# Kernel tuning notes

Measured on AMD Instinct MI355X. Metric: run time of the kernel, lower is better.

## Reference

```python
import jax, jax.numpy as jnp
import numpy as np

N = 100000
IN_DIM = 256
HID = 256
EMB = 64
E = 3200000
EPS = 1e-3  # keras BatchNormalization default epsilon


def setup_inputs() -> dict:
    key = jax.random.key(0)
    ks = jax.random.split(key, 8)
    x = jax.random.normal(ks[0], (N, IN_DIM), dtype=jnp.float32)
    edge_row = jax.random.randint(ks[1], (E,), 0, N, dtype=jnp.int32)
    edge_col = jax.random.randint(ks[2], (E,), 0, N, dtype=jnp.int32)
    edge_val = jax.random.uniform(ks[3], (E,), dtype=jnp.float32)
    # glorot-uniform weights
    lim1 = float(np.sqrt(6.0 / (IN_DIM + HID)))
    w1 = jax.random.uniform(ks[4], (IN_DIM, HID), minval=-lim1, maxval=lim1, dtype=jnp.float32)
    lim2 = float(np.sqrt(6.0 / (HID + EMB)))
    w2 = jax.random.uniform(ks[5], (HID, EMB), minval=-lim2, maxval=lim2, dtype=jnp.float32)
    # BN params (inference mode uses moving stats)
    gamma1 = jnp.ones((HID,), jnp.float32)
    beta1 = jnp.zeros((HID,), jnp.float32)
    mean1 = jax.random.normal(ks[6], (HID,), dtype=jnp.float32) * 0.1
    var1 = jnp.ones((HID,), jnp.float32)
    gamma2 = jnp.ones((EMB,), jnp.float32)
    beta2 = jnp.zeros((EMB,), jnp.float32)
    mean2 = jax.random.normal(ks[7], (EMB,), dtype=jnp.float32) * 0.1
    var2 = jnp.ones((EMB,), jnp.float32)
    return dict(x=x, edge_row=edge_row, edge_col=edge_col, edge_val=edge_val,
                w1=w1, w2=w2, gamma1=gamma1, beta1=beta1, mean1=mean1, var1=var1,
                gamma2=gamma2, beta2=beta2, mean2=mean2, var2=var2)


def _spmm(edge_row, edge_col, edge_val, dense):
    # out[i] = sum_{e: row_e == i} val_e * dense[col_e]
    gathered = edge_val[:, None] * dense[edge_col]  # [E, D]
    return jax.ops.segment_sum(gathered, edge_row, num_segments=N)


def _bn_inf(h, gamma, beta, mean, var):
    return (h - mean) * jax.lax.rsqrt(var + EPS) * gamma + beta


def reference(x, edge_row, edge_col, edge_val, w1, w2,
              gamma1, beta1, mean1, var1, gamma2, beta2, mean2, var2):
    # layer 1: A @ (X W1), BN (inference), ReLU; dropout is identity at inference
    h = _spmm(edge_row, edge_col, edge_val, x @ w1)
    h = jax.nn.relu(_bn_inf(h, gamma1, beta1, mean1, var1))
    # layer 2
    z = _spmm(edge_row, edge_col, edge_val, h @ w2)
    z = _bn_inf(z, gamma2, beta2, mean2, var2)
    return z
```

## Files before the change

kernel.cpp:

```cpp
#include <hip/hip_runtime.h>
#include <hip/hip_bf16.h>

constexpr int NN   = 100000;
constexpr int IND  = 256;
constexpr int HIDD = 256;
constexpr int EMBD = 64;
constexpr int EE   = 3200000;
constexpr int CB    = 8;
constexpr int NB    = ((NN - 1) >> CB) + 1;
constexpr int NBP   = 512;
constexpr int CHUNK = 4096;
constexpr int EPT   = CHUNK / 256;
constexpr int NCHUNK = (EE + CHUNK - 1) / CHUNK;
constexpr int GMT    = 8;
constexpr int GROWS  = GMT * 16;
constexpr int GGRID  = (NN + GROWS - 1) / GROWS;
constexpr int APITCH = 264;
#define EPS_BN 1e-3f

typedef short  short8  __attribute__((ext_vector_type(8)));
typedef float  floatx4 __attribute__((ext_vector_type(4)));
typedef float  floatx2 __attribute__((ext_vector_type(2)));

static __device__ __forceinline__ unsigned short f2bf(float f) {
  __hip_bfloat16 b = __float2bfloat16(f);
  union { __hip_bfloat16 b; unsigned short u; } cv;
  cv.b = b;
  return cv.u;
}
static __device__ __forceinline__ float bf2f(unsigned short u) {
  return __uint_as_float(((unsigned)u) << 16);
}
static __device__ __forceinline__ unsigned char f2fp8(float f) {
  return (unsigned char)__builtin_amdgcn_cvt_pk_fp8_f32(f, f, 0, false);
}

__global__ __launch_bounds__(256) void swz_w1_kernel(
    const float* __restrict__ w1, unsigned short* __restrict__ w1s) {
  const int t = blockIdx.x * blockDim.x + threadIdx.x;
  const int lane = t & 63;
  const int f = t >> 6;
  const int kt = f >> 4;
  const int nt = f & 15;
  const int n = nt * 16 + (lane & 15);
#pragma unroll
  for (int j = 0; j < 8; ++j) {
    const int k = kt * 32 + (lane >> 4) * 8 + j;
    w1s[(size_t)(f * 64 + lane) * 8 + j] = f2bf(w1[k * HIDD + n]);
  }
}

__global__ __launch_bounds__(256) void swz_w2_kernel(
    const float* __restrict__ w2, unsigned short* __restrict__ w2s) {
  const int t = blockIdx.x * blockDim.x + threadIdx.x;
  const int lane = t & 63;
  const int f = t >> 6;
  const int kt = f >> 2;
  const int nt = f & 3;
  const int n = nt * 16 + (lane & 15);
#pragma unroll
  for (int j = 0; j < 8; ++j) {
    const int k = kt * 32 + (lane >> 4) * 8 + j;
    w2s[(size_t)(f * 64 + lane) * 8 + j] = f2bf(w2[k * EMBD + n]);
  }
}

__global__ __launch_bounds__(512) void gemm1_mfma(
    const float* __restrict__ x, const unsigned short* __restrict__ w1s,
    unsigned char* __restrict__ h0) {
  __shared__ unsigned short sa[2][16][APITCH];
  const int tid  = threadIdx.x;
  const int lane = tid & 63;
  const int wave = tid >> 6;
  const int quad = lane >> 4;
  const int l15  = lane & 15;
  const short8* w1v = (const short8*)w1s;
  short8 bf[2][8];
#pragma unroll
  for (int nt2 = 0; nt2 < 2; ++nt2)
#pragma unroll
    for (int kt = 0; kt < 8; ++kt)
      bf[nt2][kt] = w1v[(size_t)(kt * 16 + wave * 2 + nt2) * 64 + lane];

  const int mbase = blockIdx.x * GROWS;
  const int srow = tid >> 5;
  const int scol = (tid & 31) * 8;

  auto srcp = [&](int mt) -> const float* {
    int r = mbase + mt * 16 + srow;
    if (r >= NN) r = NN - 1;
    return x + (size_t)r * IND + scol;
  };

  {
    const float* p = srcp(0);
    float4 g0 = *(const float4*)(p);
    float4 g1 = *(const float4*)(p + 4);
    short8 s;
    s[0] = (short)f2bf(g0.x); s[1] = (short)f2bf(g0.y);
    s[2] = (short)f2bf(g0.z); s[3] = (short)f2bf(g0.w);
    s[4] = (short)f2bf(g1.x); s[5] = (short)f2bf(g1.y);
    s[6] = (short)f2bf(g1.z); s[7] = (short)f2bf(g1.w);
    *(short8*)&sa[0][srow][(tid & 31) * 8] = s;
  }

#pragma unroll
  for (int mt = 0; mt < GMT; ++mt) {
    const int cur = mt & 1;
    float4 g0, g1;
    if (mt + 1 < GMT) {
      const float* p = srcp(mt + 1);
      g0 = *(const float4*)(p);
      g1 = *(const float4*)(p + 4);
    }
    __syncthreads();
    floatx4 c0 = {0.f, 0.f, 0.f, 0.f};
    floatx4 c1 = {0.f, 0.f, 0.f, 0.f};
#pragma unroll
    for (int kt = 0; kt < 8; ++kt) {
      short8 a = *(const short8*)&sa[cur][l15][quad * 8 + kt * 32];
      c0 = __builtin_amdgcn_mfma_f32_16x16x32_bf16(a, bf[0][kt], c0, 0, 0, 0);
      c1 = __builtin_amdgcn_mfma_f32_16x16x32_bf16(a, bf[1][kt], c1, 0, 0, 0);
    }
    const int m0 = mbase + mt * 16;
    if (m0 < NN) {
      unsigned char* o = h0 + (size_t)(m0 + quad * 4) * HIDD + wave * 32 + l15;
#pragma unroll
      for (int r = 0; r < 4; ++r) {
        o[(size_t)r * HIDD]      = f2fp8(c0[r]);
        o[(size_t)r * HIDD + 16] = f2fp8(c1[r]);
      }
    }
    if (mt + 1 < GMT) {
      short8 s;
      s[0] = (short)f2bf(g0.x); s[1] = (short)f2bf(g0.y);
      s[2] = (short)f2bf(g0.z); s[3] = (short)f2bf(g0.w);
      s[4] = (short)f2bf(g1.x); s[5] = (short)f2bf(g1.y);
      s[6] = (short)f2bf(g1.z); s[7] = (short)f2bf(g1.w);
      *(short8*)&sa[cur ^ 1][srow][(tid & 31) * 8] = s;
    }
  }
}

__global__ __launch_bounds__(256) void gemm2_mfma(
    const unsigned short* __restrict__ hb, const unsigned short* __restrict__ w2s,
    unsigned char* __restrict__ z0) {
  __shared__ unsigned short sa[2][16][APITCH];
  const int tid  = threadIdx.x;
  const int lane = tid & 63;
  const int wave = tid >> 6;
  const int quad = lane >> 4;
  const int l15  = lane & 15;
  const short8* w2v = (const short8*)w2s;
  short8 bf[8];
#pragma unroll
  for (int kt = 0; kt < 8; ++kt)
    bf[kt] = w2v[(size_t)(kt * 4 + wave) * 64 + lane];

  const int mbase = blockIdx.x * GROWS;
  const int srow = tid >> 4;
  const int scol = (tid & 15) * 16;

  auto srcp = [&](int mt) -> const unsigned short* {
    int r = mbase + mt * 16 + srow;
    if (r >= NN) r = NN - 1;
    return hb + (size_t)r * HIDD + scol;
  };

  {
    const unsigned short* p = srcp(0);
    short8 g0 = *(const short8*)(p);
    short8 g1 = *(const short8*)(p + 8);
    *(short8*)&sa[0][srow][scol]     = g0;
    *(short8*)&sa[0][srow][scol + 8] = g1;
  }

#pragma unroll
  for (int mt = 0; mt < GMT; ++mt) {
    const int cur = mt & 1;
    short8 g0, g1;
    if (mt + 1 < GMT) {
      const unsigned short* p = srcp(mt + 1);
      g0 = *(const short8*)(p);
      g1 = *(const short8*)(p + 8);
    }
    __syncthreads();
    floatx4 c = {0.f, 0.f, 0.f, 0.f};
#pragma unroll
    for (int kt = 0; kt < 8; ++kt) {
      short8 a = *(const short8*)&sa[cur][l15][quad * 8 + kt * 32];
      c = __builtin_amdgcn_mfma_f32_16x16x32_bf16(a, bf[kt], c, 0, 0, 0);
    }
    const int m0 = mbase + mt * 16;
    if (m0 < NN) {
      unsigned char* o = z0 + (size_t)(m0 + quad * 4) * EMBD + wave * 16 + l15;
#pragma unroll
      for (int r = 0; r < 4; ++r) o[(size_t)r * EMBD] = f2fp8(c[r]);
    }
    if (mt + 1 < GMT) {
      *(short8*)&sa[cur ^ 1][srow][scol]     = g0;
      *(short8*)&sa[cur ^ 1][srow][scol + 8] = g1;
    }
  }
}

__global__ __launch_bounds__(256) void histb_kernel(
    const int* __restrict__ row, int* __restrict__ bcnt) {
  __shared__ int lcnt[NB];
  for (int i = threadIdx.x; i < NB; i += 256) lcnt[i] = 0;
  __syncthreads();
  const int base = blockIdx.x * CHUNK;
  const int lim  = min(EE - base, CHUNK);
  for (int i = threadIdx.x; i < lim; i += 256)
    atomicAdd(&lcnt[row[base + i] >> CB], 1);
  __syncthreads();
  for (int i = threadIdx.x; i < NB; i += 256) {
    const int c = lcnt[i];
    if (c) atomicAdd(&bcnt[i * 16], c);
  }
}

__global__ __launch_bounds__(512) void bscan_kernel(
    const int* __restrict__ bcnt, int* __restrict__ bucket_start,
    int* __restrict__ bcur) {
  __shared__ int lds[512];
  int v = (threadIdx.x < NB) ? bcnt[threadIdx.x * 16] : 0;
  lds[threadIdx.x] = v;
  for (int off = 1; off < 512; off <<= 1) {
    __syncthreads();
    int t = (threadIdx.x >= off) ? lds[threadIdx.x - off] : 0;
    __syncthreads();
    lds[threadIdx.x] += t;
  }
  __syncthreads();
  if (threadIdx.x < NB) {
    const int excl = lds[threadIdx.x] - v;
    bucket_start[threadIdx.x] = excl;
    bcur[threadIdx.x * 16] = excl;
  }
  if (threadIdx.x == 0) bucket_start[NB] = EE;
}

__global__ __launch_bounds__(256) void partA_kernel(
    const int* __restrict__ row, const int* __restrict__ col,
    const float* __restrict__ val, int* __restrict__ bcur,
    unsigned long long* __restrict__ staged) {
  __shared__ unsigned long long sbuf[CHUNK];
  __shared__ int cnt[NBP];
  __shared__ int scn[NBP];
  __shared__ int cur[NB];
  __shared__ int gofs[NB];
  const int base = blockIdx.x * CHUNK;
  const int lim  = min(EE - base, CHUNK);
  for (int i = threadIdx.x; i < NBP; i += 256) cnt[i] = 0;
  __syncthreads();
  unsigned long long rec[EPT];
  int bkt[EPT];
#pragma unroll
  for (int j = 0; j < EPT; ++j) {
    const int idx = threadIdx.x + j * 256;
    bkt[j] = -1;
    if (idx < lim) {
      const int e = base + idx;
      const int r = row[e];
      const int c = col[e];
      const unsigned short v = f2bf(val[e]);
      rec[j] = ((unsigned long long)r << 33) | ((unsigned long long)c << 16) | v;
      bkt[j] = r >> CB;
      atomicAdd(&cnt[bkt[j]], 1);
    }
  }
  __syncthreads();
  for (int i = threadIdx.x; i < NBP; i += 256) scn[i] = cnt[i];
  __syncthreads();
  for (int off = 1; off < NBP; off <<= 1) {
    const int i0 = threadIdx.x, i1 = threadIdx.x + 256;
    const int t0 = (i0 >= off) ? scn[i0 - off] : 0;
    const int t1 = (i1 >= off) ? scn[i1 - off] : 0;
    __syncthreads();
    scn[i0] += t0;
    scn[i1] += t1;
    __syncthreads();
  }
  for (int b = threadIdx.x; b < NB; b += 256) cur[b] = scn[b] - cnt[b];
  __syncthreads();
#pragma unroll
  for (int j = 0; j < EPT; ++j)
    if (bkt[j] >= 0) {
      const int p = atomicAdd(&cur[bkt[j]], 1);
      sbuf[p] = rec[j];
    }
  __syncthreads();
  for (int b = threadIdx.x; b < NB; b += 256) {
    const int c = cnt[b];
    const int g = (c > 0) ? atomicAdd(&bcur[b * 16], c) : 0;
    gofs[b] = g - (scn[b] - c);
  }
  __syncthreads();
  for (int s = threadIdx.x; s < lim; s += 256) {
    const unsigned long long rc = sbuf[s];
    const int b = (int)(rc >> (33 + CB));
    staged[(size_t)(gofs[b] + s)] = rc;
  }
}

__global__ __launch_bounds__(256) void partB_kernel(
    const int* __restrict__ bucket_start,
    const unsigned long long* __restrict__ staged,
    int2* __restrict__ edges, int* __restrict__ row_start) {
  __shared__ int cnt[1 << CB];
  __shared__ int ofs[1 << CB];
  const int b  = blockIdx.x;
  const int r0 = b << CB;
  const int rn = min(NN - r0, 1 << CB);
  const int s  = bucket_start[b];
  const int e  = bucket_start[b + 1];
  cnt[threadIdx.x] = 0;
  __syncthreads();
  const unsigned* hi = (const unsigned*)staged;
  for (int p = s + threadIdx.x; p < e; p += 256) {
    const unsigned hw = hi[2 * p + 1];
    const int r = (int)((hw >> 1) & 0x1FFFF);
    atomicAdd(&cnt[r - r0], 1);
  }
  __syncthreads();
  const int v = cnt[threadIdx.x];
  ofs[threadIdx.x] = v;
  for (int off = 1; off < 256; off <<= 1) {
    __syncthreads();
    const int t = (threadIdx.x >= off) ? ofs[threadIdx.x - off] : 0;
    __syncthreads();
    ofs[threadIdx.x] += t;
  }
  __syncthreads();
  const int excl = ofs[threadIdx.x] - v;
  if ((int)threadIdx.x < rn) row_start[r0 + threadIdx.x] = s + excl;
  if (b == NB - 1 && threadIdx.x == 0) row_start[NN] = e;
  __syncthreads();
  cnt[threadIdx.x] = s + excl;
  __syncthreads();
  for (int p = s + threadIdx.x; p < e; p += 256) {
    const unsigned long long rc = staged[p];
    const int r = (int)(rc >> 33);
    const int c = (int)((rc >> 16) & 0x1FFFF);
    const float vv = bf2f((unsigned short)(rc & 0xFFFF));
    const int q = atomicAdd(&cnt[r - r0], 1);
    int2 pk; pk.x = c << 6; pk.y = __float_as_int(vv);
    edges[q] = pk;
  }
}

__global__ __launch_bounds__(256, 8) void spmm1_kernel(
    const unsigned char* __restrict__ h0, const int* __restrict__ row_start,
    const int2* __restrict__ edges,
    const float* __restrict__ gamma, const float* __restrict__ beta,
    const float* __restrict__ mean, const float* __restrict__ var,
    unsigned short* __restrict__ h) {
  const int row  = (blockIdx.x * blockDim.x + threadIdx.x) >> 6;
  const int lane = threadIdx.x & 63;
  const int grp  = lane >> 4;
  const int t    = lane & 15;
  const int t16  = t * 16;
  const int s = row_start[row];
  const int e = row_start[row + 1];
  floatx2 acc[8];
#pragma unroll
  for (int j = 0; j < 8; ++j) acc[j] = floatx2{0.f, 0.f};

  const int ebulk = s + ((e - s) & ~15);
  int p = s;
  for (; p < ebulk; p += 16) {
    unsigned coff[4];
    float    vv4[4];
#pragma unroll
    for (int k = 0; k < 4; ++k) {
      const int2 er = edges[p + k * 4 + grp];
      coff[k] = (unsigned)er.x;
      vv4[k]  = __int_as_float(er.y);
    }
    uint4 gg[4];
#pragma unroll
    for (int k = 0; k < 4; ++k)
      gg[k] = *(const uint4*)(h0 + (size_t)coff[k] * 4 + t16);
#pragma unroll
    for (int k = 0; k < 4; ++k) {
      const floatx2 v2 = {vv4[k], vv4[k]};
      acc[0] += __builtin_amdgcn_cvt_pk_f32_fp8(gg[k].x, false) * v2;
      acc[1] += __builtin_amdgcn_cvt_pk_f32_fp8(gg[k].x, true)  * v2;
      acc[2] += __builtin_amdgcn_cvt_pk_f32_fp8(gg[k].y, false) * v2;
      acc[3] += __builtin_amdgcn_cvt_pk_f32_fp8(gg[k].y, true)  * v2;
      acc[4] += __builtin_amdgcn_cvt_pk_f32_fp8(gg[k].z, false) * v2;
      acc[5] += __builtin_amdgcn_cvt_pk_f32_fp8(gg[k].z, true)  * v2;
      acc[6] += __builtin_amdgcn_cvt_pk_f32_fp8(gg[k].w, false) * v2;
      acc[7] += __builtin_amdgcn_cvt_pk_f32_fp8(gg[k].w, true)  * v2;
    }
  }
  for (; p < e; p += 4) {
    const int idx = p + grp;
    const bool valid = idx < e;
    const int2 er = edges[valid ? idx : e - 1];
    const unsigned coff = (unsigned)er.x;
    const float vv = valid ? __int_as_float(er.y) : 0.f;
    const uint4 gg = *(const uint4*)(h0 + (size_t)coff * 4 + t16);
    const floatx2 v2 = {vv, vv};
    acc[0] += __builtin_amdgcn_cvt_pk_f32_fp8(gg.x, false) * v2;
    acc[1] += __builtin_amdgcn_cvt_pk_f32_fp8(gg.x, true)  * v2;
    acc[2] += __builtin_amdgcn_cvt_pk_f32_fp8(gg.y, false) * v2;
    acc[3] += __builtin_amdgcn_cvt_pk_f32_fp8(gg.y, true)  * v2;
    acc[4] += __builtin_amdgcn_cvt_pk_f32_fp8(gg.z, false) * v2;
    acc[5] += __builtin_amdgcn_cvt_pk_f32_fp8(gg.z, true)  * v2;
    acc[6] += __builtin_amdgcn_cvt_pk_f32_fp8(gg.w, false) * v2;
    acc[7] += __builtin_amdgcn_cvt_pk_f32_fp8(gg.w, true)  * v2;
  }
#pragma unroll
  for (int j = 0; j < 8; ++j) {
    acc[j][0] += __shfl_xor(acc[j][0], 16);
    acc[j][1] += __shfl_xor(acc[j][1], 16);
  }
#pragma unroll
  for (int j = 0; j < 8; ++j) {
    acc[j][0] += __shfl_xor(acc[j][0], 32);
    acc[j][1] += __shfl_xor(acc[j][1], 32);
  }
  floatx2 pa, pb;
  if (grp == 0)      { pa = acc[0]; pb = acc[1]; }
  else if (grp == 1) { pa = acc[2]; pb = acc[3]; }
  else if (grp == 2) { pa = acc[4]; pb = acc[5]; }
  else               { pa = acc[6]; pb = acc[7]; }
  const int d = t16 + grp * 4;
  float4 g  = *(const float4*)(gamma + d);
  float4 b  = *(const float4*)(beta + d);
  float4 m  = *(const float4*)(mean + d);
  float4 vv = *(const float4*)(var + d);
  ushort4 o;
  o.x = f2bf(fmaxf(fmaf((pa[0] - m.x) * rsqrtf(vv.x + EPS_BN), g.x, b.x), 0.f));
  o.y = f2bf(fmaxf(fmaf((pa[1] - m.y) * rsqrtf(vv.y + EPS_BN), g.y, b.y), 0.f));
  o.z = f2bf(fmaxf(fmaf((pb[0] - m.z) * rsqrtf(vv.z + EPS_BN), g.z, b.z), 0.f));
  o.w = f2bf(fmaxf(fmaf((pb[1] - m.w) * rsqrtf(vv.w + EPS_BN), g.w, b.w), 0.f));
  *(ushort4*)(h + (size_t)row * HIDD + d) = o;
}

__global__ __launch_bounds__(256, 8) void spmm2_kernel(
    const unsigned char* __restrict__ z0, const int* __restrict__ row_start,
    const int2* __restrict__ edges,
    const float* __restrict__ gamma, const float* __restrict__ beta,
    const float* __restrict__ mean, const float* __restrict__ var,
    float* __restrict__ out) {
  const int row  = (blockIdx.x * blockDim.x + threadIdx.x) >> 6;
  const int lane = threadIdx.x & 63;
  const int grp  = lane >> 4;
  const int t    = lane & 15;
  const int t4   = t * 4;
  const int s = row_start[row];
  const int e = row_start[row + 1];
  floatx2 a01 = {0.f, 0.f};
  floatx2 a23 = {0.f, 0.f};
  const int ebulk = s + ((e - s) & ~15);
  int p = s;
  for (; p < ebulk; p += 16) {
    unsigned coff[4];
    float    vv4[4];
#pragma unroll
    for (int k = 0; k < 4; ++k) {
      const int2 er = edges[p + k * 4 + grp];
      coff[k] = (unsigned)er.x;
      vv4[k]  = __int_as_float(er.y);
    }
    unsigned gg[4];
#pragma unroll
    for (int k = 0; k < 4; ++k)
      gg[k] = *(const unsigned*)(z0 + (size_t)coff[k] + t4);
#pragma unroll
    for (int k = 0; k < 4; ++k) {
      const floatx2 v2 = {vv4[k], vv4[k]};
      a01 += __builtin_amdgcn_cvt_pk_f32_fp8(gg[k], false) * v2;
      a23 += __builtin_amdgcn_cvt_pk_f32_fp8(gg[k], true)  * v2;
    }
  }
  for (; p < e; p += 4) {
    const int idx = p + grp;
    const bool valid = idx < e;
    const int2 er = edges[valid ? idx : e - 1];
    const unsigned coff = (unsigned)er.x;
    const float vvs = valid ? __int_as_float(er.y) : 0.f;
    const unsigned gg = *(const unsigned*)(z0 + (size_t)coff + t4);
    const floatx2 v2 = {vvs, vvs};
    a01 += __builtin_amdgcn_cvt_pk_f32_fp8(gg, false) * v2;
    a23 += __builtin_amdgcn_cvt_pk_f32_fp8(gg, true)  * v2;
  }
  a01[0] += __shfl_xor(a01[0], 16); a01[1] += __shfl_xor(a01[1], 16);
  a23[0] += __shfl_xor(a23[0], 16); a23[1] += __shfl_xor(a23[1], 16);
  a01[0] += __shfl_xor(a01[0], 32); a01[1] += __shfl_xor(a01[1], 32);
  a23[0] += __shfl_xor(a23[0], 32); a23[1] += __shfl_xor(a23[1], 32);
  float av;
  if (grp == 0)      av = a01[0];
  else if (grp == 1) av = a01[1];
  else if (grp == 2) av = a23[0];
  else               av = a23[1];
  const int d = t4 + grp;
  const float r = fmaf((av - mean[d]) * rsqrtf(var[d] + EPS_BN), gamma[d],
                       beta[d]);
  out[(size_t)row * EMBD + d] = r;
}

extern "C" void kernel_launch(void* const* d_in, const int* in_sizes, int n_in,
                              void* d_out, int out_size, void* d_ws, size_t ws_size,
                              hipStream_t stream) {
  const float* x        = (const float*)d_in[0];
  const int*   edge_row = (const int*)d_in[1];
  const int*   edge_col = (const int*)d_in[2];
  const float* edge_val = (const float*)d_in[3];
  const float* w1       = (const float*)d_in[4];
  const float* w2       = (const float*)d_in[5];
  const float* gamma1   = (const float*)d_in[6];
  const float* beta1    = (const float*)d_in[7];
  const float* mean1    = (const float*)d_in[8];
  const float* var1     = (const float*)d_in[9];
  const float* gamma2   = (const float*)d_in[10];
  const float* beta2    = (const float*)d_in[11];
  const float* mean2    = (const float*)d_in[12];
  const float* var2     = (const float*)d_in[13];
  float* out = (float*)d_out;

  char* ws = (char*)d_ws;
  size_t off = 0;
  auto alloc = [&](size_t bytes) -> void* {
    void* p = ws + off;
    off = (off + bytes + 255) & ~(size_t)255;
    return p;
  };
  unsigned char*  h0  = (unsigned char*)alloc((size_t)NN * HIDD);
  unsigned short* h   = (unsigned short*)alloc((size_t)NN * HIDD * 2);
  unsigned long long* staged = (unsigned long long*)h;
  unsigned char*  z0  = (unsigned char*)alloc((size_t)NN * EMBD);
  unsigned short* w1s = (unsigned short*)alloc((size_t)IND * HIDD * 2);
  unsigned short* w2s = (unsigned short*)alloc((size_t)HIDD * EMBD * 2);
  int*   row_start    = (int*)alloc((size_t)(NN + 1) * 4);
  int*   bcnt         = (int*)alloc((size_t)NB * 16 * 4);
  int*   bcur         = (int*)alloc((size_t)NB * 16 * 4);
  int*   bucket_start = (int*)alloc((size_t)(NB + 1) * 4);
  int2*  edges        = (int2*)alloc((size_t)EE * 8);

  swz_w1_kernel<<<8192 / 256, 256, 0, stream>>>(w1, w1s);
  swz_w2_kernel<<<2048 / 256, 256, 0, stream>>>(w2, w2s);

  hipMemsetAsync(bcnt, 0, (size_t)NB * 16 * 4, stream);
  histb_kernel<<<NCHUNK, 256, 0, stream>>>(edge_row, bcnt);
  bscan_kernel<<<1, 512, 0, stream>>>(bcnt, bucket_start, bcur);
  partA_kernel<<<NCHUNK, 256, 0, stream>>>(
      edge_row, edge_col, edge_val, bcur, staged);
  partB_kernel<<<NB, 256, 0, stream>>>(bucket_start, staged, edges, row_start);

  gemm1_mfma<<<GGRID, 512, 0, stream>>>(x, w1s, h0);
  spmm1_kernel<<<NN / 4, 256, 0, stream>>>(h0, row_start, edges,
                                           gamma1, beta1, mean1, var1, h);
  gemm2_mfma<<<GGRID, 256, 0, stream>>>(h, w2s, z0);
  spmm2_kernel<<<NN / 4, 256, 0, stream>>>(z0, row_start, edges,
                                           gamma2, beta2, mean2, var2, out);
}
```

Baseline: 509.6 us.

## Build CSR with per-row global atomics instead of two-pass bucket partition

```diff
diff --git a/kernel.cpp b/kernel.cpp
--- a/kernel.cpp
+++ b/kernel.cpp
@@ -8,10 +8,6 @@
 constexpr int EE   = 3200000;
 constexpr int CB    = 8;
 constexpr int NB    = ((NN - 1) >> CB) + 1;
-constexpr int NBP   = 512;
-constexpr int CHUNK = 4096;
-constexpr int EPT   = CHUNK / 256;
-constexpr int NCHUNK = (EE + CHUNK - 1) / CHUNK;
 constexpr int GMT    = 8;
 constexpr int GROWS  = GMT * 16;
 constexpr int GGRID  = (NN + GROWS - 1) / GROWS;
@@ -27,9 +23,6 @@
   union { __hip_bfloat16 b; unsigned short u; } cv;
   cv.b = b;
   return cv.u;
-}
-static __device__ __forceinline__ float bf2f(unsigned short u) {
-  return __uint_as_float(((unsigned)u) << 16);
 }
 static __device__ __forceinline__ unsigned char f2fp8(float f) {
   return (unsigned char)__builtin_amdgcn_cvt_pk_fp8_f32(f, f, 0, false);
@@ -204,148 +197,69 @@
   }
 }
 
-__global__ __launch_bounds__(256) void histb_kernel(
-    const int* __restrict__ row, int* __restrict__ bcnt) {
-  __shared__ int lcnt[NB];
-  for (int i = threadIdx.x; i < NB; i += 256) lcnt[i] = 0;
+
+__global__ __launch_bounds__(256) void histr_kernel(
+    const int* __restrict__ row, int* __restrict__ cnt) {
+  const int i = blockIdx.x * 256 + threadIdx.x;
+  if (i < EE) atomicAdd(&cnt[row[i]], 1);
+}
+
+__global__ __launch_bounds__(256) void scanA_kernel(
+    const int* __restrict__ cnt, int* __restrict__ excl,
+    int* __restrict__ btot) {
+  __shared__ int lds[256];
+  const int r = blockIdx.x * 256 + threadIdx.x;
+  const int v = (r < NN) ? cnt[r] : 0;
+  lds[threadIdx.x] = v;
+  for (int off = 1; off < 256; off <<= 1) {
+    __syncthreads();
+    const int t = (threadIdx.x >= off) ? lds[threadIdx.x - off] : 0;
+    __syncthreads();
+    lds[threadIdx.x] += t;
+  }
   __syncthreads();
-  const int base = blockIdx.x * CHUNK;
-  const int lim  = min(EE - base, CHUNK);
-  for (int i = threadIdx.x; i < lim; i += 256)
-    atomicAdd(&lcnt[row[base + i] >> CB], 1);
-  __syncthreads();
-  for (int i = threadIdx.x; i < NB; i += 256) {
-    const int c = lcnt[i];
-    if (c) atomicAdd(&bcnt[i * 16], c);
-  }
-}
-
-__global__ __launch_bounds__(512) void bscan_kernel(
-    const int* __restrict__ bcnt, int* __restrict__ bucket_start,
-    int* __restrict__ bcur) {
+  if (r < NN) excl[r] = lds[threadIdx.x] - v;
+  if (threadIdx.x == 255) btot[blockIdx.x] = lds[255];
+}
+
+__global__ __launch_bounds__(512) void scanB_kernel(
+    const int* __restrict__ btot, int* __restrict__ bbase) {
   __shared__ int lds[512];
-  int v = (threadIdx.x < NB) ? bcnt[threadIdx.x * 16] : 0;
+  const int v = (threadIdx.x < NB) ? btot[threadIdx.x] : 0;
   lds[threadIdx.x] = v;
   for (int off = 1; off < 512; off <<= 1) {
     __syncthreads();
-    int t = (threadIdx.x >= off) ? lds[threadIdx.x - off] : 0;
+    const int t = (threadIdx.x >= off) ? lds[threadIdx.x - off] : 0;
     __syncthreads();
     lds[threadIdx.x] += t;
   }
   __syncthreads();
-  if (threadIdx.x < NB) {
-    const int excl = lds[threadIdx.x] - v;
-    bucket_start[threadIdx.x] = excl;
-    bcur[threadIdx.x * 16] = excl;
-  }
-  if (threadIdx.x == 0) bucket_start[NB] = EE;
-}
-
-__global__ __launch_bounds__(256) void partA_kernel(
+  if (threadIdx.x < NB) bbase[threadIdx.x] = lds[threadIdx.x] - v;
+}
+
+__global__ __launch_bounds__(256) void fin_kernel(
+    const int* __restrict__ bbase, const int* __restrict__ excl,
+    int* __restrict__ row_start, int* __restrict__ cursor) {
+  const int r = blockIdx.x * 256 + threadIdx.x;
+  if (r < NN) {
+    const int rs = bbase[r >> CB] + excl[r];
+    row_start[r] = rs;
+    cursor[r] = rs;
+  }
+  if (r == 0) row_start[NN] = EE;
+}
+
+__global__ __launch_bounds__(256) void scat_kernel(
     const int* __restrict__ row, const int* __restrict__ col,
-    const float* __restrict__ val, int* __restrict__ bcur,
-    unsigned long long* __restrict__ staged) {
-  __shared__ unsigned long long sbuf[CHUNK];
-  __shared__ int cnt[NBP];
-  __shared__ int scn[NBP];
-  __shared__ int cur[NB];
-  __shared__ int gofs[NB];
-  const int base = blockIdx.x * CHUNK;
-  const int lim  = min(EE - base, CHUNK);
-  for (int i = threadIdx.x; i < NBP; i += 256) cnt[i] = 0;
-  __syncthreads();
-  unsigned long long rec[EPT];
-  int bkt[EPT];
-#pragma unroll
-  for (int j = 0; j < EPT; ++j) {
-    const int idx = threadIdx.x + j * 256;
-    bkt[j] = -1;
-    if (idx < lim) {
-      const int e = base + idx;
-      const int r = row[e];
-      const int c = col[e];
-      const unsigned short v = f2bf(val[e]);
-      rec[j] = ((unsigned long long)r << 33) | ((unsigned long long)c << 16) | v;
-      bkt[j] = r >> CB;
-      atomicAdd(&cnt[bkt[j]], 1);
-    }
-  }
-  __syncthreads();
-  for (int i = threadIdx.x; i < NBP; i += 256) scn[i] = cnt[i];
-  __syncthreads();
-  for (int off = 1; off < NBP; off <<= 1) {
-    const int i0 = threadIdx.x, i1 = threadIdx.x + 256;
-    const int t0 = (i0 >= off) ? scn[i0 - off] : 0;
-    const int t1 = (i1 >= off) ? scn[i1 - off] : 0;
-    __syncthreads();
-    scn[i0] += t0;
-    scn[i1] += t1;
-    __syncthreads();
-  }
-  for (int b = threadIdx.x; b < NB; b += 256) cur[b] = scn[b] - cnt[b];
-  __syncthreads();
-#pragma unroll
-  for (int j = 0; j < EPT; ++j)
-    if (bkt[j] >= 0) {
-      const int p = atomicAdd(&cur[bkt[j]], 1);
-      sbuf[p] = rec[j];
-    }
-  __syncthreads();
-  for (int b = threadIdx.x; b < NB; b += 256) {
-    const int c = cnt[b];
-    const int g = (c > 0) ? atomicAdd(&bcur[b * 16], c) : 0;
-    gofs[b] = g - (scn[b] - c);
-  }
-  __syncthreads();
-  for (int s = threadIdx.x; s < lim; s += 256) {
-    const unsigned long long rc = sbuf[s];
-    const int b = (int)(rc >> (33 + CB));
-    staged[(size_t)(gofs[b] + s)] = rc;
-  }
-}
-
-__global__ __launch_bounds__(256) void partB_kernel(
-    const int* __restrict__ bucket_start,
-    const unsigned long long* __restrict__ staged,
-    int2* __restrict__ edges, int* __restrict__ row_start) {
-  __shared__ int cnt[1 << CB];
-  __shared__ int ofs[1 << CB];
-  const int b  = blockIdx.x;
-  const int r0 = b << CB;
-  const int rn = min(NN - r0, 1 << CB);
-  const int s  = bucket_start[b];
-  const int e  = bucket_start[b + 1];
-  cnt[threadIdx.x] = 0;
-  __syncthreads();
-  const unsigned* hi = (const unsigned*)staged;
-  for (int p = s + threadIdx.x; p < e; p += 256) {
-    const unsigned hw = hi[2 * p + 1];
-    const int r = (int)((hw >> 1) & 0x1FFFF);
-    atomicAdd(&cnt[r - r0], 1);
-  }
-  __syncthreads();
-  const int v = cnt[threadIdx.x];
-  ofs[threadIdx.x] = v;
-  for (int off = 1; off < 256; off <<= 1) {
-    __syncthreads();
-    const int t = (threadIdx.x >= off) ? ofs[threadIdx.x - off] : 0;
-    __syncthreads();
-    ofs[threadIdx.x] += t;
-  }
-  __syncthreads();
-  const int excl = ofs[threadIdx.x] - v;
-  if ((int)threadIdx.x < rn) row_start[r0 + threadIdx.x] = s + excl;
-  if (b == NB - 1 && threadIdx.x == 0) row_start[NN] = e;
-  __syncthreads();
-  cnt[threadIdx.x] = s + excl;
-  __syncthreads();
-  for (int p = s + threadIdx.x; p < e; p += 256) {
-    const unsigned long long rc = staged[p];
-    const int r = (int)(rc >> 33);
-    const int c = (int)((rc >> 16) & 0x1FFFF);
-    const float vv = bf2f((unsigned short)(rc & 0xFFFF));
-    const int q = atomicAdd(&cnt[r - r0], 1);
-    int2 pk; pk.x = c << 6; pk.y = __float_as_int(vv);
+    const float* __restrict__ val, int* __restrict__ cursor,
+    int2* __restrict__ edges) {
+  const int i = blockIdx.x * 256 + threadIdx.x;
+  if (i < EE) {
+    const int r = row[i];
+    const int q = atomicAdd(&cursor[r], 1);
+    int2 pk;
+    pk.x = col[i] << 6;
+    pk.y = __float_as_int(val[i]);
     edges[q] = pk;
   }
 }
@@ -432,12 +346,19 @@
   float4 b  = *(const float4*)(beta + d);
   float4 m  = *(const float4*)(mean + d);
   float4 vv = *(const float4*)(var + d);
-  ushort4 o;
-  o.x = f2bf(fmaxf(fmaf((pa[0] - m.x) * rsqrtf(vv.x + EPS_BN), g.x, b.x), 0.f));
-  o.y = f2bf(fmaxf(fmaf((pa[1] - m.y) * rsqrtf(vv.y + EPS_BN), g.y, b.y), 0.f));
-  o.z = f2bf(fmaxf(fmaf((pb[0] - m.z) * rsqrtf(vv.z + EPS_BN), g.z, b.z), 0.f));
-  o.w = f2bf(fmaxf(fmaf((pb[1] - m.w) * rsqrtf(vv.w + EPS_BN), g.w, b.w), 0.f));
-  *(ushort4*)(h + (size_t)row * HIDD + d) = o;
+  const unsigned short o0 =
+      f2bf(fmaxf(fmaf((pa[0] - m.x) * rsqrtf(vv.x + EPS_BN), g.x, b.x), 0.f));
+  const unsigned short o1 =
+      f2bf(fmaxf(fmaf((pa[1] - m.y) * rsqrtf(vv.y + EPS_BN), g.y, b.y), 0.f));
+  const unsigned short o2 =
+      f2bf(fmaxf(fmaf((pb[0] - m.z) * rsqrtf(vv.z + EPS_BN), g.z, b.z), 0.f));
+  const unsigned short o3 =
+      f2bf(fmaxf(fmaf((pb[1] - m.w) * rsqrtf(vv.w + EPS_BN), g.w, b.w), 0.f));
+  const unsigned long long ow =
+      (unsigned long long)o0 | ((unsigned long long)o1 << 16) |
+      ((unsigned long long)o2 << 32) | ((unsigned long long)o3 << 48);
+  __builtin_nontemporal_store(
+      ow, (unsigned long long*)(h + (size_t)row * HIDD + d));
 }
 
 __global__ __launch_bounds__(256, 8) void spmm2_kernel(
@@ -500,7 +421,7 @@
   const int d = t4 + grp;
   const float r = fmaf((av - mean[d]) * rsqrtf(var[d] + EPS_BN), gamma[d],
                        beta[d]);
-  out[(size_t)row * EMBD + d] = r;
+  __builtin_nontemporal_store(r, out + (size_t)row * EMBD + d);
 }
 
 extern "C" void kernel_launch(void* const* d_in, const int* in_sizes, int n_in,
@@ -531,25 +452,27 @@
   };
   unsigned char*  h0  = (unsigned char*)alloc((size_t)NN * HIDD);
   unsigned short* h   = (unsigned short*)alloc((size_t)NN * HIDD * 2);
-  unsigned long long* staged = (unsigned long long*)h;
   unsigned char*  z0  = (unsigned char*)alloc((size_t)NN * EMBD);
   unsigned short* w1s = (unsigned short*)alloc((size_t)IND * HIDD * 2);
   unsigned short* w2s = (unsigned short*)alloc((size_t)HIDD * EMBD * 2);
   int*   row_start    = (int*)alloc((size_t)(NN + 1) * 4);
-  int*   bcnt         = (int*)alloc((size_t)NB * 16 * 4);
-  int*   bcur         = (int*)alloc((size_t)NB * 16 * 4);
-  int*   bucket_start = (int*)alloc((size_t)(NB + 1) * 4);
+  int*   cnt          = (int*)alloc((size_t)NN * 4);
+  int*   excl         = (int*)alloc((size_t)NN * 4);
+  int*   cursor       = (int*)alloc((size_t)NN * 4);
+  int*   btot         = (int*)alloc((size_t)NB * 4);
+  int*   bbase        = (int*)alloc((size_t)NB * 4);
   int2*  edges        = (int2*)alloc((size_t)EE * 8);
 
   swz_w1_kernel<<<8192 / 256, 256, 0, stream>>>(w1, w1s);
   swz_w2_kernel<<<2048 / 256, 256, 0, stream>>>(w2, w2s);
 
-  hipMemsetAsync(bcnt, 0, (size_t)NB * 16 * 4, stream);
-  histb_kernel<<<NCHUNK, 256, 0, stream>>>(edge_row, bcnt);
-  bscan_kernel<<<1, 512, 0, stream>>>(bcnt, bucket_start, bcur);
-  partA_kernel<<<NCHUNK, 256, 0, stream>>>(
-      edge_row, edge_col, edge_val, bcur, staged);
-  partB_kernel<<<NB, 256, 0, stream>>>(bucket_start, staged, edges, row_start);
+  hipMemsetAsync(cnt, 0, (size_t)NN * 4, stream);
+  histr_kernel<<<(EE + 255) / 256, 256, 0, stream>>>(edge_row, cnt);
+  scanA_kernel<<<NB, 256, 0, stream>>>(cnt, excl, btot);
+  scanB_kernel<<<1, 512, 0, stream>>>(btot, bbase);
+  fin_kernel<<<NB, 256, 0, stream>>>(bbase, excl, row_start, cursor);
+  scat_kernel<<<(EE + 255) / 256, 256, 0, stream>>>(
+      edge_row, edge_col, edge_val, cursor, edges);
 
   gemm1_mfma<<<GGRID, 512, 0, stream>>>(x, w1s, h0);
   spmm1_kernel<<<NN / 4, 256, 0, stream>>>(h0, row_start, edges,
```

After: 790.3 us. 1.55x slower.
